# Kernel tuning notes

Hardware: AMD Instinct MI355X
Metric: run time of the kernel (lower is better)

The kernel has to match this reference:

```python
import jax, jax.numpy as jnp
import numpy as np

S, B, H = 2048, 32, 1024

def setup_inputs() -> dict:
    key = jax.random.key(0)
    k1, k2, k3, k4, k5 = jax.random.split(key, 5)
    hidden = jax.random.normal(k1, (B, H), dtype=jnp.float32)
    encoder_outputs = jax.random.normal(k2, (S, B, 2 * H), dtype=jnp.float32)
    # nn.Linear(3H, H): weight [H, 3H] in torch; store transposed [3H, H] for x @ W
    W = jax.random.normal(k3, (3 * H, H), dtype=jnp.float32) * (1.0 / np.sqrt(3 * H))
    b = jax.random.normal(k4, (H,), dtype=jnp.float32) * 0.01
    v = jax.random.uniform(k5, (H,), dtype=jnp.float32)  # torch.rand
    return {"hidden": hidden, "encoder_outputs": encoder_outputs, "W": W, "b": b, "v": v}

def reference(hidden, encoder_outputs, W, b, v):
    # hidden: [B, H]; encoder_outputs: [S, B, 2H]
    # Avoid materializing the repeated/concatenated tensor by splitting the linear:
    # cat(h_rep, enc) @ W == h @ W[:H] (broadcast over S) + enc @ W[H:]
    Wh, We = W[:H], W[H:]                         # [H, H], [2H, H]
    h_proj = hidden @ Wh + b                      # [B, H]
    energy = jnp.tanh(jnp.einsum('sbe,eh->sbh', encoder_outputs, We) + h_proj[None])  # [S, B, H]
    scores = jnp.einsum('sbh,h->bs', energy, v)   # [B, S]
    return jax.nn.softmax(scores, axis=1)
```

## Files before the change

kernel.cpp:

```cpp
#include <hip/hip_runtime.h>
#include <hip/hip_fp16.h>


typedef _Float16 half8 __attribute__((ext_vector_type(8)));
typedef float floatx4 __attribute__((ext_vector_type(4)));
typedef float f32x4 __attribute__((ext_vector_type(4)));

constexpr int SEQ = 2048;
constexpr int BAT = 32;
constexpr int HID = 1024;
constexpr int KDIM = 2048;
constexpr int MTOT = SEQ * BAT;
constexpr int KT = 64;

constexpr int B_BUF = 65536;
constexpr int A_PITCH = 64 * 16 + 16;
constexpr int A_BUF = 4 * A_PITCH;

__device__ __forceinline__ void glds16(const void* g, void* l) {
    __builtin_amdgcn_global_load_lds((__attribute__((address_space(1))) void*)(g),
                                     (__attribute__((address_space(3))) void*)(l), 16, 0, 0);
}

__global__ __launch_bounds__(256) void pack_b_kernel(const float* __restrict__ W,
                                                     _Float16* __restrict__ pb) {
    int t = blockIdx.x * blockDim.x + threadIdx.x;
    int nt = t >> 15;
    int rem = t & 32767;
    int kt = rem >> 9;
    int c = rem & 511;
    int g = c >> 7;
    int n = c & 127;
    int h = nt * 128 + n;
    int e0 = kt * 32 + g * 8;
    const float* src = W + (size_t)(1024 + e0) * 1024 + h;
    union { _Float16 hh[8]; uint4 u; } tmp;
#pragma unroll
    for (int j = 0; j < 8; ++j) tmp.hh[j] = (_Float16)src[(size_t)j * 1024];
    *(uint4*)(pb + (size_t)t * 8) = tmp.u;
}

__global__ __launch_bounds__(256) void hproj_kernel(const float* __restrict__ hidden,
                                                    const float* __restrict__ W,
                                                    const float* __restrict__ bias,
                                                    float* __restrict__ hp) {
    int b = blockIdx.x;
    int h0 = blockIdx.y * 64;
    int hl = threadIdx.x & 63;
    int ks = threadIdx.x >> 6;
    const float* hr = hidden + b * HID + ks * 256;
    const float* wc = W + (size_t)(ks * 256) * HID + h0 + hl;
    float acc = 0.0f;
#pragma unroll 8
    for (int e = 0; e < 256; ++e) acc += hr[e] * wc[(size_t)e * HID];
    __shared__ float red[256];
    red[threadIdx.x] = acc;
    __syncthreads();
    if (threadIdx.x < 64)
        hp[b * HID + h0 + threadIdx.x] = red[threadIdx.x] + red[64 + threadIdx.x] +
                                         red[128 + threadIdx.x] + red[192 + threadIdx.x] +
                                         bias[h0 + threadIdx.x];
}

__global__ __launch_bounds__(512, 2) void attn_gemm_kernel(
    const float* __restrict__ enc, const _Float16* __restrict__ pb,
    const float* __restrict__ hp, const float* __restrict__ v,
    float* __restrict__ score) {
    __shared__ char smem[2 * B_BUF + 2 * A_BUF];
    char* sB0 = smem;
    char* sB1 = smem + B_BUF;
    char* sA0 = smem + 2 * B_BUF;
    char* sA1 = smem + 2 * B_BUF + A_BUF;

    const int tid = threadIdx.x;
    const int lane = tid & 63;
    const int wv = tid >> 6;
    const int mt = blockIdx.x;
    const size_t r0 = (size_t)mt * 64;
    const int fm = lane & 15;
    const int fg = lane >> 4;

    const char* bg = (const char*)pb + (size_t)wv * KT * 8192;
    const int bl_off = wv * 8192;

    const int arow = tid >> 3;
    const int ac4 = tid & 7;
    const f32x4* agp = (const f32x4*)(enc + (r0 + arow) * KDIM) + ac4;
    const int awoff = (ac4 >> 1) * A_PITCH + arow * 16 + (ac4 & 1) * 8;

    const int ardoff = fg * A_PITCH + fm * 16;
    const int brdoff = wv * 8192 + fg * 2048 + fm * 16;

    floatx4 acc[4][8];
#pragma unroll
    for (int i = 0; i < 4; ++i)
#pragma unroll
        for (int j = 0; j < 8; ++j) acc[i][j] = (floatx4)0.0f;

    {
        const char* g = bg;
        char* l0 = sB0 + bl_off;
#pragma unroll
        for (int j = 0; j < 8; ++j)
            glds16(g + (j * 64 + lane) * 16, l0 + (j * 64 + lane) * 16);
        f32x4 f = __builtin_nontemporal_load(agp);
        union { _Float16 hh[4]; uint2 u; } pk;
        pk.hh[0] = (_Float16)f.x; pk.hh[1] = (_Float16)f.y;
        pk.hh[2] = (_Float16)f.z; pk.hh[3] = (_Float16)f.w;
        *(uint2*)(sA0 + awoff) = pk.u;
    }

    for (int kt = 0; kt < KT; ++kt) {
        const int cur = kt & 1;
        __syncthreads();
        if (kt + 1 < KT) {
            char* sBn = (cur ? sB0 : sB1);
            char* sAn = (cur ? sA0 : sA1);
            const char* g = bg + (size_t)(kt + 1) * 8192;
            char* l0 = sBn + bl_off;
#pragma unroll
            for (int j = 0; j < 8; ++j)
                glds16(g + (j * 64 + lane) * 16, l0 + (j * 64 + lane) * 16);
            f32x4 f = __builtin_nontemporal_load(agp + (kt + 1) * 8);
            union { _Float16 hh[4]; uint2 u; } pk;
            pk.hh[0] = (_Float16)f.x; pk.hh[1] = (_Float16)f.y;
            pk.hh[2] = (_Float16)f.z; pk.hh[3] = (_Float16)f.w;
            *(uint2*)(sAn + awoff) = pk.u;
        }
        const char* ab = cur ? sA1 : sA0;
        const char* bb = cur ? sB1 : sB0;
        half8 af[4];
#pragma unroll
        for (int i = 0; i < 4; ++i) af[i] = *(const half8*)(ab + ardoff + i * 256);
#pragma unroll
        for (int j = 0; j < 8; ++j) {
            half8 bf = *(const half8*)(bb + brdoff + j * 256);
#pragma unroll
            for (int i = 0; i < 4; ++i)
                acc[i][j] = __builtin_amdgcn_mfma_f32_16x16x32_f16(af[i], bf, acc[i][j], 0, 0, 0);
        }
    }

    float sums[4][4];
#pragma unroll
    for (int i = 0; i < 4; ++i)
#pragma unroll
        for (int r = 0; r < 4; ++r) sums[i][r] = 0.0f;

#pragma unroll
    for (int j = 0; j < 8; ++j) {
        int h = wv * 128 + j * 16 + fm;
        float vv = v[h];
#pragma unroll
        for (int i = 0; i < 4; ++i) {
#pragma unroll
            for (int r = 0; r < 4; ++r) {
                int row = i * 16 + fg * 4 + r;
                int b = row & 31;
                float x = acc[i][j][r] + hp[b * HID + h];
                float e2 = __expf(2.0f * x);
                float th = 1.0f - 2.0f / (e2 + 1.0f);
                sums[i][r] += th * vv;
            }
        }
    }
#pragma unroll
    for (int i = 0; i < 4; ++i)
#pragma unroll
        for (int r = 0; r < 4; ++r) {
            float s = sums[i][r];
            s += __shfl_xor(s, 1);
            s += __shfl_xor(s, 2);
            s += __shfl_xor(s, 4);
            s += __shfl_xor(s, 8);
            sums[i][r] = s;
        }
    __syncthreads();
    float* red = (float*)smem;
    if (fm == 0) {
#pragma unroll
        for (int i = 0; i < 4; ++i)
#pragma unroll
            for (int r = 0; r < 4; ++r)
                red[wv * 64 + i * 16 + fg * 4 + r] = sums[i][r];
    }
    __syncthreads();
    if (tid < 64) {
        float tot = 0.0f;
#pragma unroll
        for (int w = 0; w < 8; ++w) tot += red[w * 64 + tid];
        score[r0 + tid] = tot;
    }
}

__global__ __launch_bounds__(256) void softmax_kernel(const float* __restrict__ score,
                                                      float* __restrict__ out) {
    int b = blockIdx.x;
    int tid = threadIdx.x;
    __shared__ float redm[4];
    __shared__ float reds[4];
    float vals[8];
    float mx = -1e30f;
#pragma unroll
    for (int k = 0; k < 8; ++k) {
        int s = k * 256 + tid;
        float a = score[(size_t)s * 32 + b];
        vals[k] = a;
        mx = fmaxf(mx, a);
    }
    for (int d = 1; d < 64; d <<= 1) mx = fmaxf(mx, __shfl_xor(mx, d));
    int wv = tid >> 6;
    if ((tid & 63) == 0) redm[wv] = mx;
    __syncthreads();
    mx = fmaxf(fmaxf(redm[0], redm[1]), fmaxf(redm[2], redm[3]));
    float sum = 0.0f;
#pragma unroll
    for (int k = 0; k < 8; ++k) {
        vals[k] = __expf(vals[k] - mx);
        sum += vals[k];
    }
    for (int d = 1; d < 64; d <<= 1) sum += __shfl_xor(sum, d);
    if ((tid & 63) == 0) reds[wv] = sum;
    __syncthreads();
    sum = reds[0] + reds[1] + reds[2] + reds[3];
    float inv = 1.0f / sum;
#pragma unroll
    for (int k = 0; k < 8; ++k) out[b * SEQ + k * 256 + tid] = vals[k] * inv;
}

extern "C" void kernel_launch(void* const* d_in, const int* in_sizes, int n_in,
                              void* d_out, int out_size, void* d_ws, size_t ws_size,
                              hipStream_t stream) {
    const float* hidden = (const float*)d_in[0];
    const float* enc    = (const float*)d_in[1];
    const float* W      = (const float*)d_in[2];
    const float* bias   = (const float*)d_in[3];
    const float* v      = (const float*)d_in[4];
    float* out = (float*)d_out;

    char* ws = (char*)d_ws;
    _Float16* packB = (_Float16*)ws;
    float* hp       = (float*)(ws + (4u << 20));
    float* score    = (float*)(ws + (4u << 20) + (128u << 10));

    pack_b_kernel<<<1024, 256, 0, stream>>>(W, packB);
    hproj_kernel<<<dim3(32, 16), 256, 0, stream>>>(hidden, W, bias, hp);
    attn_gemm_kernel<<<MTOT / 64, 512, 0, stream>>>(enc, packB, hp, v, score);
    softmax_kernel<<<BAT, 256, 0, stream>>>(score, out);
}
```

Baseline: 1.066 ms.

## Hand-schedule GEMM k-loop with explicit waitcnts and deferred A conversion

Unrolls the k-loop by two with static buffer selection and replaces __syncthreads with explicit s_waitcnt vmcnt/lgkmcnt plus s_barrier, pinned in place by sched_barriers. The A-tile global load is issued before the async B loads, and its fp16 conversion and LDS store are moved after the MFMA block, so load latency can overlap compute. This aims to stop the compiler's conservative full waits from stalling each iteration. The hand-counted vmcnt(9) is fragile: if the compiler emits a different number of memory ops, the wait is wrong and could read incomplete data.

```diff
diff --git a/kernel.cpp b/kernel.cpp
--- a/kernel.cpp
+++ b/kernel.cpp
@@ -66,11 +66,10 @@
     const float* __restrict__ enc, const _Float16* __restrict__ pb,
     const float* __restrict__ hp, const float* __restrict__ v,
     float* __restrict__ score) {
-    __shared__ char smem[2 * B_BUF + 2 * A_BUF];
-    char* sB0 = smem;
-    char* sB1 = smem + B_BUF;
-    char* sA0 = smem + 2 * B_BUF;
-    char* sA1 = smem + 2 * B_BUF + A_BUF;
+    __shared__ char sB0v[B_BUF];
+    __shared__ char sB1v[B_BUF];
+    __shared__ char sA0v[A_BUF];
+    __shared__ char sA1v[A_BUF];
 
     const int tid = threadIdx.x;
     const int lane = tid & 63;
@@ -98,48 +97,72 @@
         for (int j = 0; j < 8; ++j) acc[i][j] = (floatx4)0.0f;
 
     {
+        f32x4 f = __builtin_nontemporal_load(agp);
+        __builtin_amdgcn_sched_barrier(0);
         const char* g = bg;
-        char* l0 = sB0 + bl_off;
+        char* l0 = sB0v + bl_off;
 #pragma unroll
         for (int j = 0; j < 8; ++j)
             glds16(g + (j * 64 + lane) * 16, l0 + (j * 64 + lane) * 16);
-        f32x4 f = __builtin_nontemporal_load(agp);
+        __builtin_amdgcn_sched_barrier(0);
         union { _Float16 hh[4]; uint2 u; } pk;
         pk.hh[0] = (_Float16)f.x; pk.hh[1] = (_Float16)f.y;
         pk.hh[2] = (_Float16)f.z; pk.hh[3] = (_Float16)f.w;
-        *(uint2*)(sA0 + awoff) = pk.u;
-    }
-
-    for (int kt = 0; kt < KT; ++kt) {
-        const int cur = kt & 1;
-        __syncthreads();
-        if (kt + 1 < KT) {
-            char* sBn = (cur ? sB0 : sB1);
-            char* sAn = (cur ? sA0 : sA1);
-            const char* g = bg + (size_t)(kt + 1) * 8192;
-            char* l0 = sBn + bl_off;
-#pragma unroll
-            for (int j = 0; j < 8; ++j)
-                glds16(g + (j * 64 + lane) * 16, l0 + (j * 64 + lane) * 16);
-            f32x4 f = __builtin_nontemporal_load(agp + (kt + 1) * 8);
-            union { _Float16 hh[4]; uint2 u; } pk;
-            pk.hh[0] = (_Float16)f.x; pk.hh[1] = (_Float16)f.y;
-            pk.hh[2] = (_Float16)f.z; pk.hh[3] = (_Float16)f.w;
-            *(uint2*)(sAn + awoff) = pk.u;
-        }
-        const char* ab = cur ? sA1 : sA0;
-        const char* bb = cur ? sB1 : sB0;
-        half8 af[4];
-#pragma unroll
-        for (int i = 0; i < 4; ++i) af[i] = *(const half8*)(ab + ardoff + i * 256);
-#pragma unroll
-        for (int j = 0; j < 8; ++j) {
-            half8 bf = *(const half8*)(bb + brdoff + j * 256);
-#pragma unroll
-            for (int i = 0; i < 4; ++i)
-                acc[i][j] = __builtin_amdgcn_mfma_f32_16x16x32_f16(af[i], bf, acc[i][j], 0, 0, 0);
-        }
-    }
+        *(uint2*)(sA0v + awoff) = pk.u;
+        asm volatile("s_waitcnt lgkmcnt(0)" ::: "memory");
+        __builtin_amdgcn_s_barrier();
+        __builtin_amdgcn_sched_barrier(0);
+    }
+
+#define KSTEP(KT_I, AB, BB, AN, BN, HAVE_NEXT)                                    \
+    {                                                                             \
+        f32x4 f;                                                                  \
+        if (HAVE_NEXT) {                                                          \
+            f = __builtin_nontemporal_load(agp + ((KT_I) + 1) * 8);               \
+            __builtin_amdgcn_sched_barrier(0);                                    \
+            const char* g = bg + (size_t)((KT_I) + 1) * 8192;                     \
+            char* l0 = (BN) + bl_off;                                             \
+            _Pragma("unroll")                                                     \
+            for (int j = 0; j < 8; ++j)                                           \
+                glds16(g + (j * 64 + lane) * 16, l0 + (j * 64 + lane) * 16);      \
+            __builtin_amdgcn_sched_barrier(0);                                    \
+                \
+                \
+            asm volatile("s_waitcnt vmcnt(9)" ::: "memory");                      \
+        } else {                                                                  \
+            asm volatile("s_waitcnt vmcnt(0)" ::: "memory");                      \
+        }                                                                         \
+        half8 af[4];                                                              \
+        _Pragma("unroll")                                                         \
+        for (int i = 0; i < 4; ++i)                                               \
+            af[i] = *(const half8*)((AB) + ardoff + i * 256);                     \
+        _Pragma("unroll")                                                         \
+        for (int j = 0; j < 8; ++j) {                                             \
+            half8 bf = *(const half8*)((BB) + brdoff + j * 256);                  \
+            _Pragma("unroll")                                                     \
+            for (int i = 0; i < 4; ++i)                                           \
+                acc[i][j] =                                                       \
+                    __builtin_amdgcn_mfma_f32_16x16x32_f16(af[i], bf, acc[i][j],  \
+                                                           0, 0, 0);              \
+        }                                                                         \
+        __builtin_amdgcn_sched_barrier(0);                                        \
+        if (HAVE_NEXT) {                                                          \
+            union { _Float16 hh[4]; uint2 u; } pk;      \
+            pk.hh[0] = (_Float16)f.x; pk.hh[1] = (_Float16)f.y;                   \
+            pk.hh[2] = (_Float16)f.z; pk.hh[3] = (_Float16)f.w;                   \
+            *(uint2*)((AN) + awoff) = pk.u;                                       \
+        }                                                                         \
+        asm volatile("s_waitcnt lgkmcnt(0)" ::: "memory");                        \
+        __builtin_amdgcn_s_barrier();                                             \
+        __builtin_amdgcn_sched_barrier(0);                                        \
+    }
+
+#pragma clang loop unroll(disable)
+    for (int kt2 = 0; kt2 < KT; kt2 += 2) {
+        KSTEP(kt2, sA0v, sB0v, sA1v, sB1v, true);
+        KSTEP(kt2 + 1, sA1v, sB1v, sA0v, sB0v, (kt2 + 2 < KT));
+    }
+#undef KSTEP
 
     float sums[4][4];
 #pragma unroll
@@ -176,7 +199,7 @@
             sums[i][r] = s;
         }
     __syncthreads();
-    float* red = (float*)smem;
+    float* red = (float*)sB0v;
     if (fm == 0) {
 #pragma unroll
         for (int i = 0; i < 4; ++i)
```

Result: faster. 1.017 ms (-4.7%).
